# Kernel tuning notes

Hardware: AMD Instinct MI355X
Metric: run time of the kernel (lower is better)

Reference implementation:

```python
import jax, jax.numpy as jnp
import numpy as np

DT = 0.1  # time step (forward arg dt in the torch module)


def setup_inputs() -> dict:
    key = jax.random.key(0)
    k1, k2, k3, k4 = jax.random.split(key, 4)
    B, T = 256, 100_000
    # Pre-generated 3-state Markov trajectory (the torch module generates this
    # on the host with sequential RNG; here it is a fixed int input).
    states = jax.random.randint(k1, (B, T), 0, 3).astype(jnp.int32)
    # Unit orientation vectors; entry k is the heading after the k-th tumble.
    e0s = jax.random.normal(k2, (B, T + 1, 3), dtype=jnp.float32)
    e0s = e0s / jnp.linalg.norm(e0s, axis=-1, keepdims=True)
    speed_0 = jax.random.uniform(k3, (B,), dtype=jnp.float32) * 0.001
    speed_1 = jax.random.uniform(k4, (B,), dtype=jnp.float32) * 0.005
    x0 = jnp.zeros((B, 3), jnp.float32)
    return {"states": states, "e0s": e0s, "speed_0": speed_0,
            "speed_1": speed_1, "x0": x0}


def reference(states, e0s, speed_0, speed_1, x0):
    """Vectorized equivalent of simulate_particle_trajectory (pauses=0 path).

    The per-particle while-loop with run-length segments reduces, when
    nonp_pause_type is None (pauses == 0), to:
      e0_exp[b, t] = 0                                  if states[b,t] == 2
                   = e0s[b, k(b,t)] * speed_{s}[b]       otherwise,
    where k(b,t) = number of tumbles (state==2) at steps <= t (inclusive
    cumsum: at a tumble step the output is zeroed anyway, and the step after
    the k-th tumble uses orientation e0s[k], matching the loop's k counter).
    Positions integrate the velocity: x[t] = x0 + dt * cumsum(e0_exp).
    """
    is_tumble = states == 2                                   # (B, T)
    k = jnp.cumsum(is_tumble.astype(jnp.int32), axis=1)        # (B, T)
    e0_sel = jnp.take_along_axis(e0s, k[:, :, None], axis=1)   # (B, T, 3) gather
    speed = jnp.where(states == 0, speed_0[:, None], speed_1[:, None])  # (B, T)
    vel = e0_sel * jnp.where(is_tumble, 0.0, speed)[..., None]  # e0_exp
    X = x0[:, None, :] + jnp.cumsum(vel, axis=1) * jnp.float32(DT)
    return X
```

## Files before the change

### kernel.cpp

```cpp
#include <hip/hip_runtime.h>


#define NT    256
#define IPT   8
#define CHUNK (NT * IPT)
#define NW    (NT / 64)
#define NPART 4

__device__ __forceinline__ void load_states(const int* __restrict__ st, int lim,
                                            int e0i, int out[IPT]) {
    if (e0i + IPT <= lim) {
        int4 a = *(const int4*)(st + e0i);
        int4 b = *(const int4*)(st + e0i + 4);
        out[0] = a.x; out[1] = a.y; out[2] = a.z; out[3] = a.w;
        out[4] = b.x; out[5] = b.y; out[6] = b.z; out[7] = b.w;
    } else {
        #pragma unroll
        for (int j = 0; j < IPT; ++j)
            out[j] = (e0i + j < lim) ? st[e0i + j] : 3;
    }
}

__global__ __launch_bounds__(NT)
void count_kernel(const int* __restrict__ states, int T, int psz, int npart,
                  int* __restrict__ cnt)
{
    const int blk  = blockIdx.x;
    const int b    = blk / npart;
    const int p    = blk - b * npart;
    const int tid  = threadIdx.x;
    const int lane = tid & 63;
    const int wid  = tid >> 6;

    const int* st = states + (size_t)b * T;
    const int pstart = p * psz;
    int pend = pstart + psz; if (pend > T) pend = T;

    __shared__ int s_w[NW];

    int c = 0;
    for (int base = pstart; base < pend; base += CHUNK) {
        int cur[IPT];
        load_states(st, pend, base + tid * IPT, cur);
        #pragma unroll
        for (int j = 0; j < IPT; ++j) c += (cur[j] == 2);
    }
    #pragma unroll
    for (int d = 32; d > 0; d >>= 1) c += __shfl_down(c, d, 64);
    if (lane == 0) s_w[wid] = c;
    __syncthreads();
    if (tid == 0) {
        int t = 0;
        #pragma unroll
        for (int w = 0; w < NW; ++w) t += s_w[w];
        cnt[blk] = t;
    }
}

__global__ __launch_bounds__(NT)
void velsum_kernel(const int*   __restrict__ states,
                   const float* __restrict__ e0s,
                   const float* __restrict__ sp0v,
                   const float* __restrict__ sp1v,
                   int T, int psz, int npart,
                   const int*   __restrict__ cnt,
                   float*       __restrict__ velws)
{
    const int blk  = blockIdx.x;
    const int b    = blk / npart;
    const int p    = blk - b * npart;
    const int tid  = threadIdx.x;
    const int lane = tid & 63;
    const int wid  = tid >> 6;

    const int*   st = states + (size_t)b * T;
    const float* er = e0s    + (size_t)b * (T + 1) * 3;
    const float sp0 = sp0v[b], sp1 = sp1v[b];
    const int pstart = p * psz;
    int pend = pstart + psz; if (pend > T) pend = T;

    __shared__ int   s_wi[2][NW];
    __shared__ float s_wf[NW][3];

    int kc = 0;
    for (int q = 0; q < p; ++q) kc += cnt[b * npart + q];

    float vx = 0.f, vy = 0.f, vz = 0.f;
    int par = 0;
    for (int base = pstart; base < pend; base += CHUNK, par ^= 1) {
        int cur[IPT];
        load_states(st, pend, base + tid * IPT, cur);

        int c = 0;
        #pragma unroll
        for (int j = 0; j < IPT; ++j) c += (cur[j] == 2);
        int incl = c;
        #pragma unroll
        for (int d = 1; d < 64; d <<= 1) {
            int n = __shfl_up(incl, d, 64);
            if (lane >= d) incl += n;
        }
        if (lane == 63) s_wi[par][wid] = incl;
        __syncthreads();
        int wex = 0, btot = 0;
        #pragma unroll
        for (int w = 0; w < NW; ++w) {
            int t = s_wi[par][w];
            wex  += (w < wid) ? t : 0;
            btot += t;
        }
        int k = kc + wex + (incl - c);
        #pragma unroll
        for (int j = 0; j < IPT; ++j) {
            const int s = cur[j];
            k += (s == 2);
            const float sp = (s == 0) ? sp0 : ((s == 1) ? sp1 : 0.f);
            const float* e = er + (size_t)k * 3;
            vx += e[0] * sp; vy += e[1] * sp; vz += e[2] * sp;
        }
        kc += btot;
    }

    #pragma unroll
    for (int d = 32; d > 0; d >>= 1) {
        vx += __shfl_down(vx, d, 64);
        vy += __shfl_down(vy, d, 64);
        vz += __shfl_down(vz, d, 64);
    }
    if (lane == 0) { s_wf[wid][0] = vx; s_wf[wid][1] = vy; s_wf[wid][2] = vz; }
    __syncthreads();
    if (tid == 0) {
        float tx = 0.f, ty = 0.f, tz = 0.f;
        #pragma unroll
        for (int w = 0; w < NW; ++w) {
            tx += s_wf[w][0]; ty += s_wf[w][1]; tz += s_wf[w][2];
        }
        float* o = velws + (size_t)blk * 3;
        o[0] = tx; o[1] = ty; o[2] = tz;
    }
}

__global__ __launch_bounds__(NT)
void traj_kernel(const int*   __restrict__ states,
                 const float* __restrict__ e0s,
                 const float* __restrict__ sp0v,
                 const float* __restrict__ sp1v,
                 const float* __restrict__ x0,
                 float*       __restrict__ X,
                 int T, int psz, int npart,
                 const int*   __restrict__ cnt,
                 const float* __restrict__ velws)
{
    const int blk  = blockIdx.x;
    const int b    = blk / npart;
    const int p    = blk - b * npart;
    const int tid  = threadIdx.x;
    const int lane = tid & 63;
    const int wid  = tid >> 6;

    __shared__ int   s_wi[NW];
    __shared__ float s_wf[NW][3];

    const int*   st = states + (size_t)b * T;
    const float* er = e0s    + (size_t)b * (T + 1) * 3;
    float*       xr = X      + (size_t)b * T * 3;
    const float sp0 = sp0v[b], sp1 = sp1v[b];
    const float x00 = x0[3 * b + 0], x01 = x0[3 * b + 1], x02 = x0[3 * b + 2];

    const int pstart = p * psz;
    int pend = pstart + psz; if (pend > T) pend = T;

    int   kc  = 0;
    float pcx = 0.f, pcy = 0.f, pcz = 0.f;
    for (int q = 0; q < p; ++q) {
        kc += cnt[b * npart + q];
        const float* v = velws + (size_t)(b * npart + q) * 3;
        pcx += v[0]; pcy += v[1]; pcz += v[2];
    }

    const bool al16 = (((uintptr_t)(xr + (size_t)pstart * 3)) & 15) == 0;

    int cur[IPT];
    load_states(st, pend, pstart + tid * IPT, cur);

    for (int base = pstart; base < pend; base += CHUNK) {
        int nxt[IPT];
        const bool has_next = (base + CHUNK) < pend;
        if (has_next) load_states(st, pend, base + CHUNK + tid * IPT, nxt);

        int c = 0;
        #pragma unroll
        for (int j = 0; j < IPT; ++j) c += (cur[j] == 2);
        int incl = c;
        #pragma unroll
        for (int d = 1; d < 64; d <<= 1) {
            int n = __shfl_up(incl, d, 64);
            if (lane >= d) incl += n;
        }
        if (lane == 63) s_wi[wid] = incl;
        __syncthreads();
        int wex = 0, btot = 0;
        #pragma unroll
        for (int w = 0; w < NW; ++w) {
            int t = s_wi[w];
            wex  += (w < wid) ? t : 0;
            btot += t;
        }
        int k = kc + wex + (incl - c);

        float ex[IPT], ey[IPT], ez[IPT];
        #pragma unroll
        for (int j = 0; j < IPT; ++j) {
            const int s = cur[j];
            k += (s == 2);
            const float sp = (s == 0) ? sp0 : ((s == 1) ? sp1 : 0.f);
            const float* e = er + (size_t)k * 3;
            ex[j] = e[0] * sp;
            ey[j] = e[1] * sp;
            ez[j] = e[2] * sp;
        }

        float px = 0.f, py = 0.f, pz = 0.f;
        #pragma unroll
        for (int j = 0; j < IPT; ++j) {
            px += ex[j]; ex[j] = px;
            py += ey[j]; ey[j] = py;
            pz += ez[j]; ez[j] = pz;
        }

        float ix = px, iy = py, iz = pz;
        #pragma unroll
        for (int d = 1; d < 64; d <<= 1) {
            float nx = __shfl_up(ix, d, 64);
            float ny = __shfl_up(iy, d, 64);
            float nz = __shfl_up(iz, d, 64);
            if (lane >= d) { ix += nx; iy += ny; iz += nz; }
        }
        if (lane == 63) { s_wf[wid][0] = ix; s_wf[wid][1] = iy; s_wf[wid][2] = iz; }
        __syncthreads();
        float wfx = 0.f, wfy = 0.f, wfz = 0.f, btx = 0.f, bty = 0.f, btz = 0.f;
        #pragma unroll
        for (int w = 0; w < NW; ++w) {
            float tx = s_wf[w][0], ty = s_wf[w][1], tz = s_wf[w][2];
            if (w < wid) { wfx += tx; wfy += ty; wfz += tz; }
            btx += tx; bty += ty; btz += tz;
        }
        const float bx = pcx + wfx + (ix - px);
        const float by = pcy + wfy + (iy - py);
        const float bz = pcz + wfz + (iz - pz);

        #define FX(j) (x00 + (bx + ex[j]) * 0.1f)
        #define FY(j) (x01 + (by + ey[j]) * 0.1f)
        #define FZ(j) (x02 + (bz + ez[j]) * 0.1f)
        const int e0i = base + tid * IPT;
        if (al16 && e0i + IPT <= pend) {
            float4* d4 = (float4*)(xr + (size_t)e0i * 3);
            d4[0] = make_float4(FX(0), FY(0), FZ(0), FX(1));
            d4[1] = make_float4(FY(1), FZ(1), FX(2), FY(2));
            d4[2] = make_float4(FZ(2), FX(3), FY(3), FZ(3));
            d4[3] = make_float4(FX(4), FY(4), FZ(4), FX(5));
            d4[4] = make_float4(FY(5), FZ(5), FX(6), FY(6));
            d4[5] = make_float4(FZ(6), FX(7), FY(7), FZ(7));
        } else {
            #pragma unroll
            for (int j = 0; j < IPT; ++j)
                if (e0i + j < pend) {
                    float* d = xr + (size_t)(e0i + j) * 3;
                    d[0] = FX(j); d[1] = FY(j); d[2] = FZ(j);
                }
        }
        #undef FX
        #undef FY
        #undef FZ

        kc  += btot;
        pcx += btx; pcy += bty; pcz += btz;

        #pragma unroll
        for (int j = 0; j < IPT; ++j) cur[j] = nxt[j];
    }
}

extern "C" void kernel_launch(void* const* d_in, const int* in_sizes, int n_in,
                              void* d_out, int out_size, void* d_ws, size_t ws_size,
                              hipStream_t stream) {
    const int*   states = (const int*)  d_in[0];
    const float* e0s    = (const float*)d_in[1];
    const float* sp0    = (const float*)d_in[2];
    const float* sp1    = (const float*)d_in[3];
    const float* x0     = (const float*)d_in[4];
    float*       X      = (float*)d_out;

    const int B = in_sizes[2];
    const int T = in_sizes[0] / B;

    const size_t need = (size_t)B * NPART * 16;
    if (d_ws != nullptr && ws_size >= need) {
        const int psz = (((T + NPART - 1) / NPART) + 7) & ~7;
        int*   cnt = (int*)d_ws;
        float* vel = (float*)((char*)d_ws + (size_t)B * NPART * 4);
        dim3 g(B * NPART), blk(NT);
        count_kernel <<<g, blk, 0, stream>>>(states, T, psz, NPART, cnt);
        velsum_kernel<<<g, blk, 0, stream>>>(states, e0s, sp0, sp1, T, psz, NPART,
                                             cnt, vel);
        traj_kernel  <<<g, blk, 0, stream>>>(states, e0s, sp0, sp1, x0, X, T, psz,
                                             NPART, cnt, vel);
    } else {
        const int psz = (T + 7) & ~7;
        traj_kernel<<<dim3(B), dim3(NT), 0, stream>>>(states, e0s, sp0, sp1, x0, X,
                                                      T, psz, 1, nullptr, nullptr);
    }
}
```

Before: 635.1 us.

## Fuse three-pass partitioned scan into single pass with LDS-staged orientations

Drops the count and velsum pre-passes and the 4-way per-row partitioning. Each row is now handled by one 1024-thread block that scans the whole trajectory sequentially. This removes the repeated reads of states and e0s that the extra passes needed. For every chunk, the contiguous range of orientation vectors the chunk touches is copied cooperatively into LDS so the gather reads from shared memory, with a fallback to global memory if it overflows. The risk is much less parallelism per row: only one block per row, a serial chain of chunks, and an extra barrier after the LDS copy, so the kernel may end up latency-bound instead of bandwidth-bound.

After: 612.6 us. 1.04x faster.

```diff
diff --git a/kernel.cpp b/kernel.cpp
--- a/kernel.cpp
+++ b/kernel.cpp
@@ -1,11 +1,11 @@
 #include <hip/hip_runtime.h>
 
 
-#define NT    256
-#define IPT   8
-#define CHUNK (NT * IPT)
-#define NW    (NT / 64)
-#define NPART 4
+#define NT      1024
+#define IPT     8
+#define CHUNK   (NT * IPT)
+#define NW      (NT / 64)
+#define CAPROWS 4096
 
 __device__ __forceinline__ void load_states(const int* __restrict__ st, int lim,
                                             int e0i, int out[IPT]) {
@@ -22,142 +22,20 @@
 }
 
 __global__ __launch_bounds__(NT)
-void count_kernel(const int* __restrict__ states, int T, int psz, int npart,
-                  int* __restrict__ cnt)
-{
-    const int blk  = blockIdx.x;
-    const int b    = blk / npart;
-    const int p    = blk - b * npart;
-    const int tid  = threadIdx.x;
-    const int lane = tid & 63;
-    const int wid  = tid >> 6;
-
-    const int* st = states + (size_t)b * T;
-    const int pstart = p * psz;
-    int pend = pstart + psz; if (pend > T) pend = T;
-
-    __shared__ int s_w[NW];
-
-    int c = 0;
-    for (int base = pstart; base < pend; base += CHUNK) {
-        int cur[IPT];
-        load_states(st, pend, base + tid * IPT, cur);
-        #pragma unroll
-        for (int j = 0; j < IPT; ++j) c += (cur[j] == 2);
-    }
-    #pragma unroll
-    for (int d = 32; d > 0; d >>= 1) c += __shfl_down(c, d, 64);
-    if (lane == 0) s_w[wid] = c;
-    __syncthreads();
-    if (tid == 0) {
-        int t = 0;
-        #pragma unroll
-        for (int w = 0; w < NW; ++w) t += s_w[w];
-        cnt[blk] = t;
-    }
-}
-
-__global__ __launch_bounds__(NT)
-void velsum_kernel(const int*   __restrict__ states,
-                   const float* __restrict__ e0s,
-                   const float* __restrict__ sp0v,
-                   const float* __restrict__ sp1v,
-                   int T, int psz, int npart,
-                   const int*   __restrict__ cnt,
-                   float*       __restrict__ velws)
-{
-    const int blk  = blockIdx.x;
-    const int b    = blk / npart;
-    const int p    = blk - b * npart;
-    const int tid  = threadIdx.x;
-    const int lane = tid & 63;
-    const int wid  = tid >> 6;
-
-    const int*   st = states + (size_t)b * T;
-    const float* er = e0s    + (size_t)b * (T + 1) * 3;
-    const float sp0 = sp0v[b], sp1 = sp1v[b];
-    const int pstart = p * psz;
-    int pend = pstart + psz; if (pend > T) pend = T;
-
-    __shared__ int   s_wi[2][NW];
-    __shared__ float s_wf[NW][3];
-
-    int kc = 0;
-    for (int q = 0; q < p; ++q) kc += cnt[b * npart + q];
-
-    float vx = 0.f, vy = 0.f, vz = 0.f;
-    int par = 0;
-    for (int base = pstart; base < pend; base += CHUNK, par ^= 1) {
-        int cur[IPT];
-        load_states(st, pend, base + tid * IPT, cur);
-
-        int c = 0;
-        #pragma unroll
-        for (int j = 0; j < IPT; ++j) c += (cur[j] == 2);
-        int incl = c;
-        #pragma unroll
-        for (int d = 1; d < 64; d <<= 1) {
-            int n = __shfl_up(incl, d, 64);
-            if (lane >= d) incl += n;
-        }
-        if (lane == 63) s_wi[par][wid] = incl;
-        __syncthreads();
-        int wex = 0, btot = 0;
-        #pragma unroll
-        for (int w = 0; w < NW; ++w) {
-            int t = s_wi[par][w];
-            wex  += (w < wid) ? t : 0;
-            btot += t;
-        }
-        int k = kc + wex + (incl - c);
-        #pragma unroll
-        for (int j = 0; j < IPT; ++j) {
-            const int s = cur[j];
-            k += (s == 2);
-            const float sp = (s == 0) ? sp0 : ((s == 1) ? sp1 : 0.f);
-            const float* e = er + (size_t)k * 3;
-            vx += e[0] * sp; vy += e[1] * sp; vz += e[2] * sp;
-        }
-        kc += btot;
-    }
-
-    #pragma unroll
-    for (int d = 32; d > 0; d >>= 1) {
-        vx += __shfl_down(vx, d, 64);
-        vy += __shfl_down(vy, d, 64);
-        vz += __shfl_down(vz, d, 64);
-    }
-    if (lane == 0) { s_wf[wid][0] = vx; s_wf[wid][1] = vy; s_wf[wid][2] = vz; }
-    __syncthreads();
-    if (tid == 0) {
-        float tx = 0.f, ty = 0.f, tz = 0.f;
-        #pragma unroll
-        for (int w = 0; w < NW; ++w) {
-            tx += s_wf[w][0]; ty += s_wf[w][1]; tz += s_wf[w][2];
-        }
-        float* o = velws + (size_t)blk * 3;
-        o[0] = tx; o[1] = ty; o[2] = tz;
-    }
-}
-
-__global__ __launch_bounds__(NT)
 void traj_kernel(const int*   __restrict__ states,
                  const float* __restrict__ e0s,
                  const float* __restrict__ sp0v,
                  const float* __restrict__ sp1v,
                  const float* __restrict__ x0,
                  float*       __restrict__ X,
-                 int T, int psz, int npart,
-                 const int*   __restrict__ cnt,
-                 const float* __restrict__ velws)
+                 int T)
 {
-    const int blk  = blockIdx.x;
-    const int b    = blk / npart;
-    const int p    = blk - b * npart;
+    const int b    = blockIdx.x;
     const int tid  = threadIdx.x;
     const int lane = tid & 63;
     const int wid  = tid >> 6;
 
+    __shared__ float s_e[3 * CAPROWS];
     __shared__ int   s_wi[NW];
     __shared__ float s_wf[NW][3];
 
@@ -167,26 +45,16 @@
     const float sp0 = sp0v[b], sp1 = sp1v[b];
     const float x00 = x0[3 * b + 0], x01 = x0[3 * b + 1], x02 = x0[3 * b + 2];
 
-    const int pstart = p * psz;
-    int pend = pstart + psz; if (pend > T) pend = T;
-
     int   kc  = 0;
     float pcx = 0.f, pcy = 0.f, pcz = 0.f;
-    for (int q = 0; q < p; ++q) {
-        kc += cnt[b * npart + q];
-        const float* v = velws + (size_t)(b * npart + q) * 3;
-        pcx += v[0]; pcy += v[1]; pcz += v[2];
-    }
-
-    const bool al16 = (((uintptr_t)(xr + (size_t)pstart * 3)) & 15) == 0;
 
     int cur[IPT];
-    load_states(st, pend, pstart + tid * IPT, cur);
+    load_states(st, T, tid * IPT, cur);
 
-    for (int base = pstart; base < pend; base += CHUNK) {
+    for (int base = 0; base < T; base += CHUNK) {
         int nxt[IPT];
-        const bool has_next = (base + CHUNK) < pend;
-        if (has_next) load_states(st, pend, base + CHUNK + tid * IPT, nxt);
+        const bool has_next = (base + CHUNK) < T;
+        if (has_next) load_states(st, T, base + CHUNK + tid * IPT, nxt);
 
         int c = 0;
         #pragma unroll
@@ -208,16 +76,38 @@
         }
         int k = kc + wex + (incl - c);
 
+        const int  rows    = btot + 1;
+        const bool use_lds = (rows <= CAPROWS);
+        if (use_lds) {
+            const float* ew = er + 3 * kc;
+            const int n = 3 * rows;
+            for (int idx = tid; idx < n; idx += NT) s_e[idx] = ew[idx];
+        }
+        __syncthreads();
+
         float ex[IPT], ey[IPT], ez[IPT];
-        #pragma unroll
-        for (int j = 0; j < IPT; ++j) {
-            const int s = cur[j];
-            k += (s == 2);
-            const float sp = (s == 0) ? sp0 : ((s == 1) ? sp1 : 0.f);
-            const float* e = er + (size_t)k * 3;
-            ex[j] = e[0] * sp;
-            ey[j] = e[1] * sp;
-            ez[j] = e[2] * sp;
+        if (use_lds) {
+            #pragma unroll
+            for (int j = 0; j < IPT; ++j) {
+                const int s = cur[j];
+                k += (s == 2);
+                const float sp = (s == 0) ? sp0 : ((s == 1) ? sp1 : 0.f);
+                const float* e = s_e + 3 * (k - kc);
+                ex[j] = e[0] * sp;
+                ey[j] = e[1] * sp;
+                ez[j] = e[2] * sp;
+            }
+        } else {
+            #pragma unroll
+            for (int j = 0; j < IPT; ++j) {
+                const int s = cur[j];
+                k += (s == 2);
+                const float sp = (s == 0) ? sp0 : ((s == 1) ? sp1 : 0.f);
+                const float* e = er + (size_t)k * 3;
+                ex[j] = e[0] * sp;
+                ey[j] = e[1] * sp;
+                ez[j] = e[2] * sp;
+            }
         }
 
         float px = 0.f, py = 0.f, pz = 0.f;
@@ -253,7 +143,7 @@
         #define FY(j) (x01 + (by + ey[j]) * 0.1f)
         #define FZ(j) (x02 + (bz + ez[j]) * 0.1f)
         const int e0i = base + tid * IPT;
-        if (al16 && e0i + IPT <= pend) {
+        if (e0i + IPT <= T) {
             float4* d4 = (float4*)(xr + (size_t)e0i * 3);
             d4[0] = make_float4(FX(0), FY(0), FZ(0), FX(1));
             d4[1] = make_float4(FY(1), FZ(1), FX(2), FY(2));
@@ -264,7 +154,7 @@
         } else {
             #pragma unroll
             for (int j = 0; j < IPT; ++j)
-                if (e0i + j < pend) {
+                if (e0i + j < T) {
                     float* d = xr + (size_t)(e0i + j) * 3;
                     d[0] = FX(j); d[1] = FY(j); d[2] = FZ(j);
                 }
@@ -294,20 +184,5 @@
     const int B = in_sizes[2];
     const int T = in_sizes[0] / B;
 
-    const size_t need = (size_t)B * NPART * 16;
-    if (d_ws != nullptr && ws_size >= need) {
-        const int psz = (((T + NPART - 1) / NPART) + 7) & ~7;
-        int*   cnt = (int*)d_ws;
-        float* vel = (float*)((char*)d_ws + (size_t)B * NPART * 4);
-        dim3 g(B * NPART), blk(NT);
-        count_kernel <<<g, blk, 0, stream>>>(states, T, psz, NPART, cnt);
-        velsum_kernel<<<g, blk, 0, stream>>>(states, e0s, sp0, sp1, T, psz, NPART,
-                                             cnt, vel);
-        traj_kernel  <<<g, blk, 0, stream>>>(states, e0s, sp0, sp1, x0, X, T, psz,
-                                             NPART, cnt, vel);
-    } else {
-        const int psz = (T + 7) & ~7;
-        traj_kernel<<<dim3(B), dim3(NT), 0, stream>>>(states, e0s, sp0, sp1, x0, X,
-                                                      T, psz, 1, nullptr, nullptr);
-    }
+    traj_kernel<<<dim3(B), dim3(NT), 0, stream>>>(states, e0s, sp0, sp1, x0, X, T);
 }
```
